# Kernel optimization log

Measured on AMD Instinct MI355X. Metric: run time of the kernel, lower is better.

The kernel has to match this reference:

```python
import jax, jax.numpy as jnp
import numpy as np

B, H, W, D, C = 2, 128, 128, 8, 64
HEADS, DIM_HEAD = 4, 16
F_IN = C * D            # 512
F_OUT = DIM_HEAD * HEADS * D  # 512


def setup_inputs() -> dict:
    key = jax.random.key(0)
    ks = jax.random.split(key, 8)
    s = 0.02
    return {
        "x_in": jax.random.normal(ks[0], (B, H, W, D, C), dtype=jnp.float32),
        "Wq": jax.random.normal(ks[1], (F_IN, F_OUT), dtype=jnp.float32) * s,
        "Wk": jax.random.normal(ks[2], (F_IN, F_OUT), dtype=jnp.float32) * s,
        "Wv": jax.random.normal(ks[3], (F_IN, F_OUT), dtype=jnp.float32) * s,
        "rescale": jnp.ones((HEADS, 1, 1), dtype=jnp.float32),
        "Wp": jax.random.normal(ks[4], (F_OUT, F_IN), dtype=jnp.float32) * s,
        "bp": jnp.zeros((F_IN,), dtype=jnp.float32),
        "pos_w1": jax.random.normal(ks[5], (C, 1, 3, 3, 3), dtype=jnp.float32) * s,
        "pos_w2": jax.random.normal(ks[6], (C, 1, 3, 3, 3), dtype=jnp.float32) * s,
    }


def _dwconv3d(y, kern, groups):
    # y: [b,c,d,h,w], kern: [c,1,3,3,3] depthwise
    return jax.lax.conv_general_dilated(
        y, kern, window_strides=(1, 1, 1), padding="SAME",
        feature_group_count=groups,
        dimension_numbers=("NCDHW", "OIDHW", "NCDHW"))


def reference(x_in, Wq, Wk, Wv, rescale, Wp, bp, pos_w1, pos_w2):
    b, h, w, d, c = x_in.shape
    heads = rescale.shape[0]
    n = h * w
    x = x_in.reshape(b, n, d * c)
    q_inp = x @ Wq
    k_inp = x @ Wk
    v_inp = x @ Wv

    def split(t):  # [b,n,heads*Dh] -> [b,heads,Dh,n]  (Dh = dim_head*num_frm)
        return t.reshape(b, n, heads, -1).transpose(0, 2, 3, 1)

    q, k, v = split(q_inp), split(k_inp), split(v_inp)
    # L2-normalize along spatial axis n (last dim), torch F.normalize eps=1e-12
    q = q / jnp.maximum(jnp.linalg.norm(q, axis=-1, keepdims=True), 1e-12)
    k = k / jnp.maximum(jnp.linalg.norm(k, axis=-1, keepdims=True), 1e-12)
    # channel attention: [b,heads,Dh,Dh]
    attn = jnp.einsum("bhdn,bhen->bhde", k, q) * rescale
    attn = jax.nn.softmax(attn, axis=-1)
    out = jnp.einsum("bhde,bhen->bhdn", attn, v)  # [b,heads,Dh,n]
    out = out.transpose(0, 3, 1, 2).reshape(b, n, -1)  # [b,n,heads*Dh]
    out_c = (out @ Wp + bp).reshape(b, h, w, d, c)

    # positional branch: depthwise conv3d over [b,c,d,h,w]
    vp = v_inp.reshape(b, h, w, d, c).transpose(0, 4, 3, 1, 2)
    p = _dwconv3d(vp, pos_w1, c)
    p = jax.nn.gelu(p, approximate=False)
    p = _dwconv3d(p, pos_w2, c)
    out_p = p.transpose(0, 3, 4, 2, 1)  # -> [b,h,w,d,c]
    return out_c + out_p
```

## Files before the change

kernel.cpp:

```cpp
#include <hip/hip_runtime.h>
#include <math.h>
#include <stdint.h>


using short8  = __attribute__((ext_vector_type(8))) short;
using f32x4   = __attribute__((ext_vector_type(4))) float;

__device__ __forceinline__ float bf2f(unsigned short u) {
  union { unsigned int i; float f; } v; v.i = ((unsigned int)u) << 16; return v.f;
}
__device__ __forceinline__ unsigned short f2bf(float f) {
  union { float f; unsigned int i; } v; v.f = f;
  unsigned int r = v.i + 0x7fffu + ((v.i >> 16) & 1u);
  return (unsigned short)(r >> 16);
}

__device__ __forceinline__ void g2l16(const void* g, void* l) {
  __builtin_amdgcn_global_load_lds(
      (__attribute__((address_space(1))) void*)(unsigned long long)(uintptr_t)g,
      (__attribute__((address_space(3))) void*)(unsigned int)(uintptr_t)l,
      16, 0, 0);
}

__device__ __forceinline__ float fast_gelu(float x) {
  float y = fabsf(x) * 0.70710678118654752f;
  float t = __builtin_amdgcn_rcpf(1.0f + 0.3275911f * y);
  float p = ((((1.061405429f * t - 1.453152027f) * t + 1.421413741f) * t
              - 0.284496736f) * t + 0.254829592f) * t;
  float er = 1.0f - p * __expf(-y * y);
  er = copysignf(er, x);
  return 0.5f * x * (1.0f + er);
}

__global__ __launch_bounds__(256) void convert_x(const float* __restrict__ x,
                                                 unsigned short* __restrict__ xb) {
  int i = (blockIdx.x * 256 + threadIdx.x) * 8;
  float4 a = *(const float4*)&x[i];
  float4 b = *(const float4*)&x[i + 4];
  ushort4 o0, o1;
  o0.x = f2bf(a.x); o0.y = f2bf(a.y); o0.z = f2bf(a.z); o0.w = f2bf(a.w);
  o1.x = f2bf(b.x); o1.y = f2bf(b.y); o1.z = f2bf(b.z); o1.w = f2bf(b.w);
  uint4 o; 
  o.x = *(unsigned*)&o0.x; o.y = *(unsigned*)&o0.z;
  o.z = *(unsigned*)&o1.x; o.w = *(unsigned*)&o1.z;
  *(uint4*)&xb[i] = o;
}

__global__ __launch_bounds__(256) void prep_w(const float* __restrict__ Wq,
                                              const float* __restrict__ Wk,
                                              const float* __restrict__ Wv,
                                              const float* __restrict__ Wp,
                                              unsigned short* __restrict__ Wcat_t,
                                              unsigned short* __restrict__ Wp_t) {
  __shared__ unsigned short Ls[32 * 36];
  int bid = blockIdx.x;
  int mat = bid >> 8, tile = bid & 255;
  int tr = (tile >> 4) * 32, tc = (tile & 15) * 32;
  const float* src = (mat == 0) ? Wq : (mat == 1) ? Wk : (mat == 2) ? Wv : Wp;
  int t = threadIdx.x;
  int r = t >> 3, c4 = (t & 7) * 4;
  float4 v = *(const float4*)&src[(tr + r) * 512 + tc + c4];
  Ls[(c4 + 0) * 36 + r] = f2bf(v.x);
  Ls[(c4 + 1) * 36 + r] = f2bf(v.y);
  Ls[(c4 + 2) * 36 + r] = f2bf(v.z);
  Ls[(c4 + 3) * 36 + r] = f2bf(v.w);
  __syncthreads();
  int rn = t >> 3, ck4 = (t & 7) * 4;
  ushort4 o;
  o.x = Ls[rn * 36 + ck4 + 0]; o.y = Ls[rn * 36 + ck4 + 1];
  o.z = Ls[rn * 36 + ck4 + 2]; o.w = Ls[rn * 36 + ck4 + 3];
  unsigned short* dst = (mat < 3)
      ? &Wcat_t[(long)(mat * 512 + tc + rn) * 512 + tr + ck4]
      : &Wp_t[(long)(tc + rn) * 512 + tr + ck4];
  *(ushort4*)dst = o;
}

__global__ __launch_bounds__(256, 2) void qk_gram(
    const unsigned short* __restrict__ x_bf,
    const unsigned short* __restrict__ Wcat_t,
    float* __restrict__ Gp, float* __restrict__ ss) {
  __shared__ unsigned short sh[38912];
  const int mt2 = blockIdx.x, h = blockIdx.y, b = blockIdx.z;
  const int t = threadIdx.x;
  const int lane = t & 63, w = t >> 6;
  const int wm = w >> 1, wn = w & 1;
  const int quad = lane >> 4, l16 = lane & 15;
  const int sr2 = lane >> 2, sc2 = lane & 3;
  const unsigned short* Bq = Wcat_t + (long)(h * 128) * 512;
  const unsigned short* Bk = Wcat_t + (long)(512 + h * 128) * 512;

  f32x4 g[4][4] = {};

  for (int half = 0; half < 2; half++) {
    const unsigned short* A = x_bf + ((long)b * 16384 + (mt2 * 2 + half) * 128) * 512;
    f32x4 aq[4][4] = {}, ak[4][4] = {};

    auto stage = [&](int k0, int d) {
      unsigned short* Sa = sh + d * 12288;
      unsigned short* Sq = Sa + 4096;
      unsigned short* Sk = Sa + 8192;
#pragma unroll
      for (int q = 0; q < 2; q++) {
        int r = q * 64 + w * 16 + sr2;
        int ca = (sc2 ^ (sr2 & 3)) * 8;
        long off = (long)r * 512 + k0 + ca;
        int ldsb = (q * 64 + w * 16) * 32;
        g2l16(&A[off],  &Sa[ldsb]);
        g2l16(&Bq[off], &Sq[ldsb]);
        g2l16(&Bk[off], &Sk[ldsb]);
      }
    };

    stage(0, 0);
    __syncthreads();
    for (int ks = 0; ks < 16; ks++) {
      int d = ks & 1;
      if (ks < 15) stage((ks + 1) * 32, d ^ 1);
      const unsigned short* Sa = sh + d * 12288;
      const unsigned short* Sq = Sa + 4096;
      const unsigned short* Sk = Sa + 8192;
      short8 af[4], bq4[4], bk4[4];
#pragma unroll
      for (int i = 0; i < 4; i++) {
        int r = wm * 64 + i * 16 + l16;
        int s = quad ^ (r & 3);
        af[i] = *(const short8*)&Sa[r * 32 + s * 8];
      }
#pragma unroll
      for (int j = 0; j < 4; j++) {
        int r = wn * 64 + j * 16 + l16;
        int s = quad ^ (r & 3);
        bq4[j] = *(const short8*)&Sq[r * 32 + s * 8];
        bk4[j] = *(const short8*)&Sk[r * 32 + s * 8];
      }
#pragma unroll
      for (int i = 0; i < 4; i++)
#pragma unroll
        for (int j = 0; j < 4; j++) {
          aq[i][j] = __builtin_amdgcn_mfma_f32_16x16x32_bf16(af[i], bq4[j], aq[i][j], 0, 0, 0);
          ak[i][j] = __builtin_amdgcn_mfma_f32_16x16x32_bf16(af[i], bk4[j], ak[i][j], 0, 0, 0);
        }
      __syncthreads();
    }

    unsigned short* kT = sh;
    unsigned short* qT = sh + 17408;
    float* red = (float*)(sh + 34816);
#pragma unroll
    for (int i = 0; i < 4; i++) {
      int mm = wm * 64 + i * 16 + quad * 4;
#pragma unroll
      for (int j = 0; j < 4; j++) {
        int f = wn * 64 + j * 16 + l16;
        ushort4 oq = { f2bf(aq[i][j][0]), f2bf(aq[i][j][1]), f2bf(aq[i][j][2]), f2bf(aq[i][j][3]) };
        ushort4 ok = { f2bf(ak[i][j][0]), f2bf(ak[i][j][1]), f2bf(ak[i][j][2]), f2bf(ak[i][j][3]) };
        *(ushort4*)&qT[f * 136 + mm] = oq;
        *(ushort4*)&kT[f * 136 + mm] = ok;
      }
    }
    int grp = wm * 4 + quad;
#pragma unroll
    for (int j = 0; j < 4; j++) {
      float pq = 0.f, pk = 0.f;
#pragma unroll
      for (int i = 0; i < 4; i++)
#pragma unroll
        for (int r = 0; r < 4; r++) { pq += aq[i][j][r] * aq[i][j][r]; pk += ak[i][j][r] * ak[i][j][r]; }
      int col = wn * 64 + j * 16 + l16;
      red[grp * 128 + col] = pq;
      red[1024 + grp * 128 + col] = pk;
    }
    __syncthreads();
#pragma unroll
    for (int kk2 = 0; kk2 < 4; kk2++) {
      short8 afk[4], bfq[4];
#pragma unroll
      for (int i = 0; i < 4; i++)
        afk[i] = *(const short8*)&kT[(wm * 64 + i * 16 + l16) * 136 + kk2 * 32 + quad * 8];
#pragma unroll
      for (int j = 0; j < 4; j++)
        bfq[j] = *(const short8*)&qT[(wn * 64 + j * 16 + l16) * 136 + kk2 * 32 + quad * 8];
#pragma unroll
      for (int i = 0; i < 4; i++)
#pragma unroll
        for (int j = 0; j < 4; j++)
          g[i][j] = __builtin_amdgcn_mfma_f32_16x16x32_bf16(afk[i], bfq[j], g[i][j], 0, 0, 0);
    }
    {
      int sel = t >> 7, col = t & 127;
      float s = 0.f;
#pragma unroll
      for (int g2 = 0; g2 < 8; g2++) s += red[sel * 1024 + g2 * 128 + col];
      atomicAdd(&ss[b * 1024 + sel * 512 + h * 128 + col], s);
    }
    __syncthreads();
  }

  float* gp = Gp + (((long)(b * 64 + mt2) * 4 + h) << 14);
#pragma unroll
  for (int i = 0; i < 4; i++) {
    int dd = wm * 64 + i * 16 + quad * 4;
#pragma unroll
    for (int j = 0; j < 4; j++) {
      int e = wn * 64 + j * 16 + l16;
      *(f32x4*)&gp[e * 128 + dd] = g[i][j];
    }
  }
}

__global__ __launch_bounds__(256, 3) void v_gemm(
    const unsigned short* __restrict__ x_bf,
    const unsigned short* __restrict__ Wcat_t,
    unsigned short* __restrict__ v) {
  __shared__ unsigned short As[8192];
  __shared__ unsigned short Bs[8192];
  const int mt = blockIdx.x, nt = blockIdx.y, b = blockIdx.z;
  const int t = threadIdx.x;
  const int lane = t & 63, w = t >> 6;
  const int wm = w >> 1, wn = w & 1;
  const int quad = lane >> 4, l16 = lane & 15;
  const int sr = lane >> 3, sc = lane & 7;
  const unsigned short* A  = x_bf + ((long)b * 16384 + mt * 128) * 512;
  const unsigned short* Bt = Wcat_t + (long)(1024 + nt * 128) * 512;

  f32x4 acc[4][4] = {};
  for (int k0 = 0; k0 < 512; k0 += 64) {
#pragma unroll
    for (int q = 0; q < 4; q++) {
      int r = q * 32 + w * 8 + sr;
      int ca = (sc ^ sr) * 8;
      g2l16(&A[(long)r * 512 + k0 + ca],  &As[(q * 32 + w * 8) * 64]);
      g2l16(&Bt[(long)r * 512 + k0 + ca], &Bs[(q * 32 + w * 8) * 64]);
    }
    __syncthreads();
#pragma unroll
    for (int kk = 0; kk < 2; kk++) {
      short8 af[4], bf[4];
#pragma unroll
      for (int i = 0; i < 4; i++) {
        int r = wm * 64 + i * 16 + l16;
        int s = (kk * 4 + quad) ^ (r & 7);
        af[i] = *(const short8*)&As[r * 64 + s * 8];
      }
#pragma unroll
      for (int j = 0; j < 4; j++) {
        int r = wn * 64 + j * 16 + l16;
        int s = (kk * 4 + quad) ^ (r & 7);
        bf[j] = *(const short8*)&Bs[r * 64 + s * 8];
      }
#pragma unroll
      for (int i = 0; i < 4; i++)
#pragma unroll
        for (int j = 0; j < 4; j++)
          acc[i][j] = __builtin_amdgcn_mfma_f32_16x16x32_bf16(bf[j], af[i], acc[i][j], 0, 0, 0);
    }
    __syncthreads();
  }
  unsigned short* vout = v + ((long)b * 16384 + mt * 128) * 512 + nt * 128;
#pragma unroll
  for (int i = 0; i < 4; i++) {
    long rbase = (long)(wm * 64 + i * 16 + l16) * 512;
#pragma unroll
    for (int j = 0; j < 4; j++) {
      int col = wn * 64 + j * 16 + quad * 4;
      uint2 o;
      o.x = (unsigned)f2bf(acc[i][j][0]) | ((unsigned)f2bf(acc[i][j][1]) << 16);
      o.y = (unsigned)f2bf(acc[i][j][2]) | ((unsigned)f2bf(acc[i][j][3]) << 16);
      *(uint2*)&vout[rbase + col] = o;
    }
  }
}

__global__ __launch_bounds__(256) void reduce_g(const float* __restrict__ Gp,
                                                float* __restrict__ G) {
  int i = blockIdx.x * 256 + threadIdx.x;
  int b = i >> 16, h = (i >> 14) & 3, r = i & 16383;
  const float* p = Gp + (((long)b * 256 + h) << 14) + r;
  float s = 0.f;
#pragma unroll 8
  for (int mtv = 0; mtv < 64; mtv++) s += p[(long)mtv * 65536];
  G[i] = s;
}

__global__ __launch_bounds__(256) void softmax_kernel(const float* __restrict__ Gt,
                                                      const float* __restrict__ ss,
                                                      const float* __restrict__ rescale,
                                                      unsigned short* __restrict__ Abd) {
  __shared__ float L[128 * 129];
  __shared__ float rsq[128];
  __shared__ float rsk[128];
  int h = blockIdx.x, b = blockIdx.y;
  int t = threadIdx.x;
  const float* g = Gt + (long)(b * 4 + h) * 16384;
  if (t < 128) rsq[t] = rsqrtf(fmaxf(ss[b * 1024 + h * 128 + t], 1e-24f));
  else { int d = t - 128; rsk[d] = rsqrtf(fmaxf(ss[b * 1024 + 512 + h * 128 + d], 1e-24f)); }
  __syncthreads();
  float rs = rescale[h];
  for (int i = t; i < 16384; i += 256) {
    int e = i >> 7, d = i & 127;
    L[d * 129 + e] = g[i] * rsk[d] * rsq[e] * rs;
  }
  __syncthreads();
  if (t < 128) {
    float* row = &L[t * 129];
    float mx = -1e30f;
    for (int e = 0; e < 128; e++) mx = fmaxf(mx, row[e]);
    float sum = 0.0f;
    for (int e = 0; e < 128; e++) { float ex = __expf(row[e] - mx); row[e] = ex; sum += ex; }
    float inv = 1.0f / sum;
    long abase = (long)b * 262144;
    for (int e = 0; e < 128; e++)
      Abd[abase + (long)(h * 128 + e) * 512 + h * 128 + t] = f2bf(row[e] * inv);
  }
}

__global__ __launch_bounds__(256, 3) void gemm_lds(
    const unsigned short* __restrict__ A, const unsigned short* __restrict__ Bt,
    unsigned short* __restrict__ C, const float* __restrict__ bias,
    int lda, int ldb, int ldc, int K, long sA, long sB, long sC) {
  __shared__ unsigned short As[128 * 64];
  __shared__ unsigned short Bs[128 * 64];
  const int t = threadIdx.x;
  const int m0 = blockIdx.x * 128, n0 = blockIdx.y * 128;
  A  += (long)blockIdx.z * sA + (long)m0 * lda;
  Bt += (long)blockIdx.z * sB + (long)n0 * ldb;
  C  += (long)blockIdx.z * sC;
  const int lane = t & 63, w = t >> 6;
  const int wm = w >> 1, wn = w & 1;
  const int quad = lane >> 4, l16 = lane & 15;
  const int sr = lane >> 3, sc = lane & 7;

  f32x4 acc[4][4] = {};

  for (int k0 = 0; k0 < K; k0 += 64) {
#pragma unroll
    for (int q = 0; q < 4; q++) {
      int r = q * 32 + w * 8 + sr;
      int ca = (sc ^ sr) * 8;
      g2l16(&A[(long)r * lda + k0 + ca], &As[(q * 32 + w * 8) * 64]);
      g2l16(&Bt[(long)r * ldb + k0 + ca], &Bs[(q * 32 + w * 8) * 64]);
    }
    __syncthreads();
#pragma unroll
    for (int kk = 0; kk < 2; kk++) {
      short8 af[4], bfq[4];
#pragma unroll
      for (int i = 0; i < 4; i++) {
        int r = wm * 64 + i * 16 + l16;
        int s = (kk * 4 + quad) ^ (r & 7);
        af[i] = *(const short8*)&As[r * 64 + s * 8];
      }
#pragma unroll
      for (int j = 0; j < 4; j++) {
        int r = wn * 64 + j * 16 + l16;
        int s = (kk * 4 + quad) ^ (r & 7);
        bfq[j] = *(const short8*)&Bs[r * 64 + s * 8];
      }
#pragma unroll
      for (int i = 0; i < 4; i++)
#pragma unroll
        for (int j = 0; j < 4; j++)
          acc[i][j] = __builtin_amdgcn_mfma_f32_16x16x32_bf16(bfq[j], af[i], acc[i][j], 0, 0, 0);
    }
    __syncthreads();
  }

#pragma unroll
  for (int i = 0; i < 4; i++) {
    long rbase = (long)(m0 + wm * 64 + i * 16 + l16) * ldc;
#pragma unroll
    for (int j = 0; j < 4; j++) {
      int col = n0 + wn * 64 + j * 16 + quad * 4;
      float b0 = 0.f, b1 = 0.f, b2 = 0.f, b3 = 0.f;
      if (bias) { float4 bv = *(const float4*)&bias[col]; b0 = bv.x; b1 = bv.y; b2 = bv.z; b3 = bv.w; }
      uint2 o;
      o.x = (unsigned)f2bf(acc[i][j][0] + b0) | ((unsigned)f2bf(acc[i][j][1] + b1) << 16);
      o.y = (unsigned)f2bf(acc[i][j][2] + b2) | ((unsigned)f2bf(acc[i][j][3] + b3) << 16);
      *(uint2*)&C[rbase + col] = o;
    }
  }
}

template <bool GELU>
__global__ __launch_bounds__(256, 4) void dwconv_kernel(
    const unsigned short* __restrict__ in,
    const float* __restrict__ wgt,
    const unsigned short* __restrict__ addc,
    unsigned short* __restrict__ outb,
    float* __restrict__ outf) {
  __shared__ float wl[27 * 64];
  int t = threadIdx.x;
  for (int i = t; i < 1728; i += 256) {
    int c = i / 27, tap = i % 27;
    wl[tap * 64 + c] = wgt[i];
  }
  __syncthreads();
  int h = blockIdx.y, b = blockIdx.z;
  int fg = t & 63, q = t >> 6;
  int w0 = blockIdx.x * 16 + q * 4;
  int f0 = fg * 8;
  int d = f0 >> 6, cch = f0 & 63;

  float acc[4][8] = {};
#pragma unroll
  for (int kh = 0; kh < 3; kh++) {
    int gh = h + kh - 1;
    if ((unsigned)gh >= 128u) continue;
    long rbase = (long)(b * 16384 + gh * 128);
#pragma unroll
    for (int kd = 0; kd < 3; kd++) {
      int dz = d + kd - 1;
      if ((unsigned)dz >= 8u) continue;
      int fz = dz * 64 + cch;
      float wv[3][8];
#pragma unroll
      for (int kw = 0; kw < 3; kw++) {
        int tap = kd * 9 + kh * 3 + kw;
        *(float4*)&wv[kw][0] = *(const float4*)&wl[tap * 64 + cch];
        *(float4*)&wv[kw][4] = *(const float4*)&wl[tap * 64 + cch + 4];
      }
      uint4 rr[6];
#pragma unroll
      for (int cc = 0; cc < 6; cc++) {
        int gw = w0 + cc - 1;
        uint4 vv = {0u, 0u, 0u, 0u};
        if ((unsigned)gw < 128u)
          vv = *(const uint4*)&in[(rbase + gw) * 512 + fz];
        rr[cc] = vv;
      }
#pragma unroll
      for (int cc = 0; cc < 6; cc++) {
        const unsigned short* u = (const unsigned short*)&rr[cc];
        float tf[8];
#pragma unroll
        for (int j = 0; j < 8; j++) tf[j] = bf2f(u[j]);
#pragma unroll
        for (int kw = 0; kw < 3; kw++) {
          int s = cc - kw;
          if (s < 0 || s > 3) continue;
#pragma unroll
          for (int j = 0; j < 8; j++) acc[s][j] += tf[j] * wv[kw][j];
        }
      }
    }
  }
#pragma unroll
  for (int s = 0; s < 4; s++) {
    long row = (long)(b * 16384 + h * 128 + (w0 + s));
    if (GELU) {
      unsigned short o[8];
#pragma unroll
      for (int j = 0; j < 8; j++) o[j] = f2bf(fast_gelu(acc[s][j]));
      *(uint4*)&outb[row * 512 + f0] = *(uint4*)&o[0];
    } else {
      uint4 av = *(const uint4*)&addc[row * 512 + f0];
      const unsigned short* au = (const unsigned short*)&av;
      float o[8];
#pragma unroll
      for (int j = 0; j < 8; j++) o[j] = acc[s][j] + bf2f(au[j]);
      *(float4*)&outf[row * 512 + f0]     = *(float4*)&o[0];
      *(float4*)&outf[row * 512 + f0 + 4] = *(float4*)&o[4];
    }
  }
}

extern "C" void kernel_launch(void* const* d_in, const int* in_sizes, int n_in,
                              void* d_out, int out_size, void* d_ws, size_t ws_size,
                              hipStream_t stream) {
  const float* x   = (const float*)d_in[0];
  const float* Wq  = (const float*)d_in[1];
  const float* Wk  = (const float*)d_in[2];
  const float* Wv  = (const float*)d_in[3];
  const float* rsc = (const float*)d_in[4];
  const float* Wp  = (const float*)d_in[5];
  const float* bp  = (const float*)d_in[6];
  const float* pw1 = (const float*)d_in[7];
  const float* pw2 = (const float*)d_in[8];
  float* out = (float*)d_out;

  char* ws = (char*)d_ws;
  unsigned short* x_bf   = (unsigned short*)(ws + 0);
  unsigned short* v      = (unsigned short*)(ws + 33554432);
  unsigned short* out_c  = (unsigned short*)(ws + 67108864);
  float*          Gp     = (float*)(ws + 100663296);
  unsigned short* Wcat_t = (unsigned short*)(ws + 167772160);
  unsigned short* Wp_t   = (unsigned short*)(ws + 169345024);
  float*          ss     = (float*)(ws + 169869312);
  float*          G      = (float*)(ws + 169877504);
  unsigned short* Abd    = (unsigned short*)(ws + 170401792);
  unsigned short* Mt     = (unsigned short*)(ws + 171450368);
  unsigned short* p1     = x_bf;

  hipMemsetAsync(ss, 0, 8192, stream);
  hipMemsetAsync(Abd, 0, 1048576, stream);

  convert_x<<<8192, 256, 0, stream>>>(x, x_bf);
  prep_w<<<1024, 256, 0, stream>>>(Wq, Wk, Wv, Wp, Wcat_t, Wp_t);

  qk_gram<<<dim3(64, 4, 2), 256, 0, stream>>>(x_bf, Wcat_t, Gp, ss);
  v_gemm<<<dim3(128, 4, 2), 256, 0, stream>>>(x_bf, Wcat_t, v);

  reduce_g<<<512, 256, 0, stream>>>(Gp, G);
  softmax_kernel<<<dim3(4, 2, 1), 256, 0, stream>>>(G, ss, rsc, Abd);

  gemm_lds<<<dim3(4, 4, 2), 256, 0, stream>>>(
      Wp_t, Abd, Mt, nullptr, 512, 512, 512, 512, 0L, 262144L, 262144L);

  gemm_lds<<<dim3(128, 4, 2), 256, 0, stream>>>(
      v, Mt, out_c, bp, 512, 512, 512, 512,
      (long)16384 * 512, 262144L, (long)16384 * 512);

  dwconv_kernel<true><<<dim3(8, 128, 2), 256, 0, stream>>>(
      v, pw1, nullptr, p1, nullptr);
  dwconv_kernel<false><<<dim3(8, 128, 2), 256, 0, stream>>>(
      p1, pw2, out_c, nullptr, out);
}
```

Before: 351.6 us.

## Replace double-buffered k32 staging with single-buffered k64 tiles in qk_gram

The Gram kernel's K loop now stages 64-wide K tiles into a single LDS buffer with an 8-way XOR swizzle, instead of double-buffering 32-wide tiles. This halves the number of loop iterations and barrier pairs per tile. In exchange it loses the overlap between async global-to-LDS loads and the MFMA work, because each tile is loaded and synchronized before compute starts.

```diff
diff --git a/kernel.cpp b/kernel.cpp
--- a/kernel.cpp
+++ b/kernel.cpp
@@ -80,12 +80,15 @@
     const unsigned short* __restrict__ Wcat_t,
     float* __restrict__ Gp, float* __restrict__ ss) {
   __shared__ unsigned short sh[38912];
+  unsigned short* As = sh;
+  unsigned short* B0 = sh + 8192;
+  unsigned short* B1 = sh + 16384;
   const int mt2 = blockIdx.x, h = blockIdx.y, b = blockIdx.z;
   const int t = threadIdx.x;
   const int lane = t & 63, w = t >> 6;
   const int wm = w >> 1, wn = w & 1;
   const int quad = lane >> 4, l16 = lane & 15;
-  const int sr2 = lane >> 2, sc2 = lane & 3;
+  const int sr = lane >> 3, sc = lane & 7;
   const unsigned short* Bq = Wcat_t + (long)(h * 128) * 512;
   const unsigned short* Bk = Wcat_t + (long)(512 + h * 128) * 512;
 
@@ -94,55 +97,42 @@
   for (int half = 0; half < 2; half++) {
     const unsigned short* A = x_bf + ((long)b * 16384 + (mt2 * 2 + half) * 128) * 512;
     f32x4 aq[4][4] = {}, ak[4][4] = {};
-
-    auto stage = [&](int k0, int d) {
-      unsigned short* Sa = sh + d * 12288;
-      unsigned short* Sq = Sa + 4096;
-      unsigned short* Sk = Sa + 8192;
-#pragma unroll
-      for (int q = 0; q < 2; q++) {
-        int r = q * 64 + w * 16 + sr2;
-        int ca = (sc2 ^ (sr2 & 3)) * 8;
-        long off = (long)r * 512 + k0 + ca;
-        int ldsb = (q * 64 + w * 16) * 32;
-        g2l16(&A[off],  &Sa[ldsb]);
-        g2l16(&Bq[off], &Sq[ldsb]);
-        g2l16(&Bk[off], &Sk[ldsb]);
-      }
-    };
-
-    stage(0, 0);
-    __syncthreads();
-    for (int ks = 0; ks < 16; ks++) {
-      int d = ks & 1;
-      if (ks < 15) stage((ks + 1) * 32, d ^ 1);
-      const unsigned short* Sa = sh + d * 12288;
-      const unsigned short* Sq = Sa + 4096;
-      const unsigned short* Sk = Sa + 8192;
-      short8 af[4], bq4[4], bk4[4];
-#pragma unroll
-      for (int i = 0; i < 4; i++) {
-        int r = wm * 64 + i * 16 + l16;
-        int s = quad ^ (r & 3);
-        af[i] = *(const short8*)&Sa[r * 32 + s * 8];
-      }
-#pragma unroll
-      for (int j = 0; j < 4; j++) {
-        int r = wn * 64 + j * 16 + l16;
-        int s = quad ^ (r & 3);
-        bq4[j] = *(const short8*)&Sq[r * 32 + s * 8];
-        bk4[j] = *(const short8*)&Sk[r * 32 + s * 8];
-      }
-#pragma unroll
-      for (int i = 0; i < 4; i++)
+    for (int k0 = 0; k0 < 512; k0 += 64) {
+#pragma unroll
+      for (int q = 0; q < 4; q++) {
+        int r = q * 32 + w * 8 + sr;
+        int ca = (sc ^ sr) * 8;
+        g2l16(&A[(long)r * 512 + k0 + ca],  &As[(q * 32 + w * 8) * 64]);
+        g2l16(&Bq[(long)r * 512 + k0 + ca], &B0[(q * 32 + w * 8) * 64]);
+        g2l16(&Bk[(long)r * 512 + k0 + ca], &B1[(q * 32 + w * 8) * 64]);
+      }
+      __syncthreads();
+#pragma unroll
+      for (int kk = 0; kk < 2; kk++) {
+        short8 af[4], bq[4], bk[4];
+#pragma unroll
+        for (int i = 0; i < 4; i++) {
+          int r = wm * 64 + i * 16 + l16;
+          int s = (kk * 4 + quad) ^ (r & 7);
+          af[i] = *(const short8*)&As[r * 64 + s * 8];
+        }
 #pragma unroll
         for (int j = 0; j < 4; j++) {
-          aq[i][j] = __builtin_amdgcn_mfma_f32_16x16x32_bf16(af[i], bq4[j], aq[i][j], 0, 0, 0);
-          ak[i][j] = __builtin_amdgcn_mfma_f32_16x16x32_bf16(af[i], bk4[j], ak[i][j], 0, 0, 0);
+          int r = wn * 64 + j * 16 + l16;
+          int s = (kk * 4 + quad) ^ (r & 7);
+          bq[j] = *(const short8*)&B0[r * 64 + s * 8];
+          bk[j] = *(const short8*)&B1[r * 64 + s * 8];
         }
+#pragma unroll
+        for (int i = 0; i < 4; i++)
+#pragma unroll
+          for (int j = 0; j < 4; j++) {
+            aq[i][j] = __builtin_amdgcn_mfma_f32_16x16x32_bf16(af[i], bq[j], aq[i][j], 0, 0, 0);
+            ak[i][j] = __builtin_amdgcn_mfma_f32_16x16x32_bf16(af[i], bk[j], ak[i][j], 0, 0, 0);
+          }
+      }
       __syncthreads();
     }
-
     unsigned short* kT = sh;
     unsigned short* qT = sh + 17408;
     float* red = (float*)(sh + 34816);
```

Measured after the change: 347.6 us. No clear change (-1.2%).
